# Performance work log

Hardware: AMD Instinct MI355X
Metric: run time of the kernel (lower is better)

Reference implementation:

```python
import jax, jax.numpy as jnp
import numpy as np

N, F, E, LIN, C, B = 16384, 500, 128, 128, 10, 4096
P_EDGE = 0.002  # ~32 avg degree


def _l2norm(x):
    # F.normalize(dim=1), eps=1e-12
    n = jnp.linalg.norm(x, axis=1, keepdims=True)
    return x / jnp.maximum(n, 1e-12)


def setup_inputs() -> dict:
    key = jax.random.key(0)
    ks = jax.random.split(key, 10)
    adj = (jax.random.uniform(ks[0], (N, N)) < P_EDGE).astype(jnp.float32)
    idx = jnp.arange(N)
    adj = adj.at[idx, idx].set(1.0)  # self-loops guarantee degree >= 1
    data = jax.random.normal(ks[1], (N, F), dtype=jnp.float32)
    nodes = jax.random.randint(ks[2], (B,), 0, N)
    # Encoder 1: Linear(2F -> E); Encoder 2: Linear(2E -> E); classifier heads
    W1 = jax.random.normal(ks[3], (E, 2 * F), dtype=jnp.float32) * 0.03
    b1 = jnp.zeros((E,), jnp.float32)
    W2 = jax.random.normal(ks[4], (E, 2 * E), dtype=jnp.float32) * 0.06
    b2 = jnp.zeros((E,), jnp.float32)
    Wl1 = jax.random.normal(ks[5], (LIN, E), dtype=jnp.float32) * 0.08
    bl1 = jnp.zeros((LIN,), jnp.float32)
    Wl2 = jax.random.normal(ks[6], (C, LIN), dtype=jnp.float32) * 0.12
    bl2 = jnp.zeros((C,), jnp.float32)
    return {"nodes": nodes, "adj": adj, "data": data,
            "W1": W1, "b1": b1, "W2": W2, "b2": b2,
            "Wl1": Wl1, "bl1": bl1, "Wl2": Wl2, "bl2": bl2}


def reference(nodes, adj, data, W1, b1, W2, b2, Wl1, bl1, Wl2, bl2):
    deg = jnp.sum(adj, axis=1, keepdims=True)  # [N,1]
    # Layer 1 (mean aggregator over full neighbor set): computed for all nodes
    neigh1 = (adj @ data) / deg                               # [N,F]
    h1 = jnp.concatenate([data, neigh1], axis=1)              # [N,2F] (self, neigh)
    H1 = _l2norm(jax.nn.relu(h1 @ W1.T + b1))                 # [N,E]
    # Layer 2: only for the queried node batch
    neigh2 = (adj[nodes] @ H1) / deg[nodes]                   # [B,E]
    h2 = jnp.concatenate([H1[nodes], neigh2], axis=1)         # [B,2E]
    H2 = _l2norm(jax.nn.relu(h2 @ W2.T + b2))                 # [B,E]
    x = H2 @ Wl1.T + bl1                                      # [B,LIN]
    x = x @ Wl2.T + bl2                                       # [B,C]
    return jax.nn.softmax(x, axis=1)
```

## Files before the change

### kernel.cpp

```cpp
#include <hip/hip_runtime.h>
#include <math.h>
#include <stddef.h>

#define N_NODES 16384
#define F_DIM   500
#define E_DIM   128
#define C_DIM   10
#define B_DIM   4096
#define MAXDEG  128

__global__ void k_prep_w1(const float* __restrict__ W1, float* __restrict__ W1s) {
    int idx = blockIdx.x * 256 + threadIdx.x;
    int e = idx & 255, k = idx >> 8;
    W1s[idx] = W1[(size_t)(e & 127) * 1000 + (e >> 7) * 500 + k];
}
__global__ void k_prep_w2(const float* __restrict__ W2, float* __restrict__ W2s) {
    int idx = blockIdx.x * 256 + threadIdx.x;
    int e = idx & 255, k = idx >> 8;
    W2s[idx] = W2[(size_t)(e & 127) * 256 + (e >> 7) * 128 + k];
}
__global__ void k_prep_wl1(const float* __restrict__ Wl1, float* __restrict__ Wl1t) {
    int idx = blockIdx.x * 256 + threadIdx.x;
    int e = idx & 127, k = idx >> 7;
    Wl1t[idx] = Wl1[(size_t)e * 128 + k];
}

__global__ __launch_bounds__(256) void k_gemm_s(const float* __restrict__ A, int K,
                                                const float* __restrict__ Bs,
                                                float* __restrict__ Cout) {
    __shared__ float sAT[32][36];
    __shared__ float sW[32][256];
    const int tid = threadIdx.x;
    const int c0 = (tid & 31) * 4;
    const int r0 = (tid >> 5) * 4;
    const int blockM = blockIdx.x * 32;
    const int kk_s = tid & 31;
    const int mm_s = tid >> 5;
    float acc[4][8] = {};

    for (int k0 = 0; k0 < K; k0 += 32) {
#pragma unroll
        for (int r = 0; r < 4; ++r) {
            int m = mm_s + r * 8;
            int k = k0 + kk_s;
            sAT[kk_s][m] = (k < K) ? A[(size_t)(blockM + m) * K + k] : 0.0f;
        }
#pragma unroll
        for (int q = 0; q < 8; ++q) {
            int idx4 = tid + 256 * q;
            int row = idx4 >> 6;
            int e4 = idx4 & 63;
            float4 w;
            if (k0 + row < K) w = ((const float4*)(Bs + (size_t)(k0 + row) * 256))[e4];
            else              w = make_float4(0.f, 0.f, 0.f, 0.f);
            *(float4*)&sW[row][e4 * 4] = w;
        }
        __syncthreads();
#pragma unroll 8
        for (int kk = 0; kk < 32; ++kk) {
            float4 a4 = *(const float4*)&sAT[kk][r0];
            float4 w0 = *(const float4*)&sW[kk][c0];
            float4 w1 = *(const float4*)&sW[kk][c0 + 128];
            float av[4] = {a4.x, a4.y, a4.z, a4.w};
            float wv[8] = {w0.x, w0.y, w0.z, w0.w, w1.x, w1.y, w1.z, w1.w};
#pragma unroll
            for (int i = 0; i < 4; ++i)
#pragma unroll
                for (int j = 0; j < 8; ++j)
                    acc[i][j] += av[i] * wv[j];
        }
        __syncthreads();
    }
#pragma unroll
    for (int i = 0; i < 4; ++i) {
        size_t base = (size_t)(blockM + r0 + i) * 256;
        *(float4*)&Cout[base + c0]       = make_float4(acc[i][0], acc[i][1], acc[i][2], acc[i][3]);
        *(float4*)&Cout[base + c0 + 128] = make_float4(acc[i][4], acc[i][5], acc[i][6], acc[i][7]);
    }
}

__global__ __launch_bounds__(256) void k_agg1(const float* __restrict__ adj,
                                              const float* __restrict__ X,
                                              const float* __restrict__ b1,
                                              float* __restrict__ H1,
                                              int* __restrict__ nbr,
                                              int* __restrict__ deg) {
    const int i = blockIdx.x;
    const int t = threadIdx.x;
    const float4* row4 = (const float4*)(adj + (size_t)i * N_NODES);
    __shared__ int s_cnt;
    __shared__ int s_idx[MAXDEG];
    __shared__ float s_part[2][128];
    __shared__ float s_w[2];
    if (t == 0) s_cnt = 0;
    __syncthreads();
    float4 v[16];
#pragma unroll
    for (int p = 0; p < 16; ++p) v[p] = row4[p * 256 + t];
#pragma unroll
    for (int p = 0; p < 16; ++p) {
        int col = p * 1024 + t * 4;
        if (v[p].x != 0.f) { int q = atomicAdd(&s_cnt, 1); if (q < MAXDEG) s_idx[q] = col;     }
        if (v[p].y != 0.f) { int q = atomicAdd(&s_cnt, 1); if (q < MAXDEG) s_idx[q] = col + 1; }
        if (v[p].z != 0.f) { int q = atomicAdd(&s_cnt, 1); if (q < MAXDEG) s_idx[q] = col + 2; }
        if (v[p].w != 0.f) { int q = atomicAdd(&s_cnt, 1); if (q < MAXDEG) s_idx[q] = col + 3; }
    }
    __syncthreads();
    int cnt = s_cnt; if (cnt > MAXDEG) cnt = MAXDEG;
    if (t < cnt) nbr[(size_t)i * MAXDEG + t] = s_idx[t];
    if (t == 0) deg[i] = cnt;
    const float inv = 1.0f / (float)cnt;
    const int col = t & 127;
    const int g = t >> 7;
    float acc = 0.f;
    for (int k = g; k < cnt; k += 2)
        acc += X[(size_t)s_idx[k] * 256 + 128 + col];
    s_part[g][col] = acc;
    __syncthreads();
    float vv = 0.f;
    if (t < 128) {
        float tot = s_part[0][t] + s_part[1][t];
        vv = X[(size_t)i * 256 + t] + tot * inv + b1[t];
        vv = fmaxf(vv, 0.f);
        float s = vv * vv;
#pragma unroll
        for (int off = 32; off > 0; off >>= 1) s += __shfl_down(s, off, 64);
        if ((t & 63) == 0) s_w[t >> 6] = s;
    }
    __syncthreads();
    if (t < 128) {
        float denom = fmaxf(sqrtf(s_w[0] + s_w[1]), 1e-12f);
        H1[(size_t)i * 128 + t] = vv / denom;
    }
}

__global__ __launch_bounds__(128) void k_l2head(const int* __restrict__ nodes,
                                                const int* __restrict__ nbr,
                                                const int* __restrict__ deg,
                                                const float* __restrict__ Y,
                                                const float* __restrict__ b2,
                                                const float* __restrict__ Wl1t,
                                                const float* __restrict__ bl1,
                                                const float* __restrict__ Wl2,
                                                const float* __restrict__ bl2,
                                                float* __restrict__ out) {
    const int b = blockIdx.x;
    const int t = threadIdx.x;
    const int n = nodes[b];
    const int cnt = deg[n];
    __shared__ int s_idx[MAXDEG];
    __shared__ float s_h[128];
    __shared__ float s_x[128];
    __shared__ float s_c[C_DIM];
    __shared__ float s_w[2];
    if (t < cnt) s_idx[t] = nbr[(size_t)n * MAXDEG + t];
    __syncthreads();
    float a0 = 0.f, a1 = 0.f;
    int k = 0;
    for (; k + 1 < cnt; k += 2) {
        a0 += Y[(size_t)s_idx[k]     * 256 + 128 + t];
        a1 += Y[(size_t)s_idx[k + 1] * 256 + 128 + t];
    }
    if (k < cnt) a0 += Y[(size_t)s_idx[k] * 256 + 128 + t];
    float vv = Y[(size_t)n * 256 + t] + (a0 + a1) / (float)cnt + b2[t];
    vv = fmaxf(vv, 0.f);
    float s = vv * vv;
#pragma unroll
    for (int off = 32; off > 0; off >>= 1) s += __shfl_down(s, off, 64);
    if ((t & 63) == 0) s_w[t >> 6] = s;
    __syncthreads();
    float denom = fmaxf(sqrtf(s_w[0] + s_w[1]), 1e-12f);
    s_h[t] = vv / denom;
    __syncthreads();
    float x1 = bl1[t];
#pragma unroll 8
    for (int kk = 0; kk < 128; ++kk)
        x1 += Wl1t[kk * 128 + t] * s_h[kk];
    s_x[t] = x1;
    __syncthreads();
    if (t < C_DIM) {
        float l = bl2[t];
        const float* wr = Wl2 + (size_t)t * 128;
        for (int kk = 0; kk < 128; ++kk) l += wr[kk] * s_x[kk];
        s_c[t] = l;
    }
    __syncthreads();
    if (t < C_DIM) {
        float mx = -1e30f;
        for (int c = 0; c < C_DIM; ++c) mx = fmaxf(mx, s_c[c]);
        float se = 0.f;
        for (int c = 0; c < C_DIM; ++c) se += expf(s_c[c] - mx);
        out[(size_t)b * C_DIM + t] = expf(s_c[t] - mx) / se;
    }
}

extern "C" void kernel_launch(void* const* d_in, const int* in_sizes, int n_in,
                              void* d_out, int out_size, void* d_ws, size_t ws_size,
                              hipStream_t stream) {
    const int*   nodes = (const int*)  d_in[0];
    const float* adj   = (const float*)d_in[1];
    const float* data  = (const float*)d_in[2];
    const float* W1    = (const float*)d_in[3];
    const float* b1    = (const float*)d_in[4];
    const float* W2    = (const float*)d_in[5];
    const float* b2    = (const float*)d_in[6];
    const float* Wl1   = (const float*)d_in[7];
    const float* bl1   = (const float*)d_in[8];
    const float* Wl2   = (const float*)d_in[9];
    const float* bl2   = (const float*)d_in[10];
    float* out = (float*)d_out;

    float* ws = (float*)d_ws;
    float* W1s  = ws;
    float* W2s  = W1s  + 128000;
    float* Wl1t = W2s  + 32768;
    float* X    = Wl1t + 16384;
    float* H1   = X    + 4194304;
    float* Y    = H1   + 2097152;
    int*   nbr  = (int*)(Y + 4194304);
    int*   deg  = nbr  + 16384 * MAXDEG;

    k_prep_w1 <<<500, 256, 0, stream>>>(W1, W1s);
    k_prep_w2 <<<128, 256, 0, stream>>>(W2, W2s);
    k_prep_wl1<<<64,  256, 0, stream>>>(Wl1, Wl1t);

    k_gemm_s<<<N_NODES / 32, 256, 0, stream>>>(data, F_DIM, W1s, X);
    k_agg1  <<<N_NODES, 256, 0, stream>>>(adj, X, b1, H1, nbr, deg);

    k_gemm_s<<<N_NODES / 32, 256, 0, stream>>>(H1, E_DIM, W2s, Y);
    k_l2head<<<B_DIM, 128, 0, stream>>>(nodes, nbr, deg, Y, b2, Wl1t, bl1, Wl2, bl2, out);
}
```

Measured before the change: 1.530 ms.

## Register-prefetch GEMM with larger 64-row tiles and tiled weight transposes

The weight-shuffle prep kernels are replaced by a shared-memory tiled transpose kernel launched per weight slice, so both reads and writes are coalesced. The shared GEMM now computes 64 rows per block with an 8x8 per-thread tile. It prefetches the next K chunk into registers while computing the current one, hiding global load latency behind FMAs. This raises register pressure and halves the block count.

```diff
diff --git a/kernel.cpp b/kernel.cpp
--- a/kernel.cpp
+++ b/kernel.cpp
@@ -9,70 +9,97 @@
 #define B_DIM   4096
 #define MAXDEG  128
 
-__global__ void k_prep_w1(const float* __restrict__ W1, float* __restrict__ W1s) {
-    int idx = blockIdx.x * 256 + threadIdx.x;
-    int e = idx & 255, k = idx >> 8;
-    W1s[idx] = W1[(size_t)(e & 127) * 1000 + (e >> 7) * 500 + k];
-}
-__global__ void k_prep_w2(const float* __restrict__ W2, float* __restrict__ W2s) {
-    int idx = blockIdx.x * 256 + threadIdx.x;
-    int e = idx & 255, k = idx >> 8;
-    W2s[idx] = W2[(size_t)(e & 127) * 256 + (e >> 7) * 128 + k];
-}
-__global__ void k_prep_wl1(const float* __restrict__ Wl1, float* __restrict__ Wl1t) {
-    int idx = blockIdx.x * 256 + threadIdx.x;
-    int e = idx & 127, k = idx >> 7;
-    Wl1t[idx] = Wl1[(size_t)e * 128 + k];
+__global__ void k_tp(const float* __restrict__ src, float* __restrict__ dst,
+                     int srcStride, int cOff, int Kc, int eOff, int dstStride) {
+    __shared__ float tile[32][33];
+    const int k0 = blockIdx.x * 32;
+    const int e0 = blockIdx.y * 32;
+    const int tx = threadIdx.x, ty0 = threadIdx.y;
+#pragma unroll
+    for (int q = 0; q < 4; ++q) {
+        int ty = ty0 + q * 8;
+        int k = k0 + tx;
+        tile[ty][tx] = (k < Kc) ? src[(size_t)(e0 + ty) * srcStride + cOff + k] : 0.0f;
+    }
+    __syncthreads();
+#pragma unroll
+    for (int q = 0; q < 4; ++q) {
+        int ty = ty0 + q * 8;
+        int k = k0 + ty;
+        if (k < Kc) dst[(size_t)k * dstStride + eOff + e0 + tx] = tile[tx][ty];
+    }
 }
 
 __global__ __launch_bounds__(256) void k_gemm_s(const float* __restrict__ A, int K,
                                                 const float* __restrict__ Bs,
                                                 float* __restrict__ Cout) {
-    __shared__ float sAT[32][36];
+    __shared__ float sAT[32][68];
     __shared__ float sW[32][256];
     const int tid = threadIdx.x;
     const int c0 = (tid & 31) * 4;
-    const int r0 = (tid >> 5) * 4;
-    const int blockM = blockIdx.x * 32;
+    const int r0 = (tid >> 5) * 8;
+    const int blockM = blockIdx.x * 64;
     const int kk_s = tid & 31;
-    const int mm_s = tid >> 5;
-    float acc[4][8] = {};
-
-    for (int k0 = 0; k0 < K; k0 += 32) {
-#pragma unroll
-        for (int r = 0; r < 4; ++r) {
-            int m = mm_s + r * 8;
-            int k = k0 + kk_s;
-            sAT[kk_s][m] = (k < K) ? A[(size_t)(blockM + m) * K + k] : 0.0f;
-        }
+    const int mg_s = (tid >> 5) * 8;
+    float acc[8][8] = {};
+    float  pa[8];
+    float4 pw[8];
+
+    const int nch = (K + 31) >> 5;
+
+    auto loadG = [&](int k0) {
+        int k = k0 + kk_s;
+#pragma unroll
+        for (int r = 0; r < 8; ++r)
+            pa[r] = (k < K) ? A[(size_t)(blockM + mg_s + r) * K + k] : 0.0f;
 #pragma unroll
         for (int q = 0; q < 8; ++q) {
             int idx4 = tid + 256 * q;
-            int row = idx4 >> 6;
-            int e4 = idx4 & 63;
-            float4 w;
-            if (k0 + row < K) w = ((const float4*)(Bs + (size_t)(k0 + row) * 256))[e4];
-            else              w = make_float4(0.f, 0.f, 0.f, 0.f);
-            *(float4*)&sW[row][e4 * 4] = w;
-        }
-        __syncthreads();
+            int row = idx4 >> 6, e4 = idx4 & 63;
+            pw[q] = (k0 + row < K) ? ((const float4*)(Bs + (size_t)(k0 + row) * 256))[e4]
+                                   : make_float4(0.f, 0.f, 0.f, 0.f);
+        }
+    };
+    auto storeL = [&]() {
+#pragma unroll
+        for (int r = 0; r < 8; ++r) sAT[kk_s][mg_s + r] = pa[r];
+#pragma unroll
+        for (int q = 0; q < 8; ++q) {
+            int idx4 = tid + 256 * q;
+            int row = idx4 >> 6, e4 = idx4 & 63;
+            *(float4*)&sW[row][e4 * 4] = pw[q];
+        }
+    };
+
+    loadG(0);
+    storeL();
+    __syncthreads();
+
+    for (int c = 1; c <= nch; ++c) {
+        const bool more = (c < nch);
+        if (more) loadG(c * 32);
 #pragma unroll 8
         for (int kk = 0; kk < 32; ++kk) {
-            float4 a4 = *(const float4*)&sAT[kk][r0];
+            float4 a0 = *(const float4*)&sAT[kk][r0];
+            float4 a1 = *(const float4*)&sAT[kk][r0 + 4];
             float4 w0 = *(const float4*)&sW[kk][c0];
             float4 w1 = *(const float4*)&sW[kk][c0 + 128];
-            float av[4] = {a4.x, a4.y, a4.z, a4.w};
+            float av[8] = {a0.x, a0.y, a0.z, a0.w, a1.x, a1.y, a1.z, a1.w};
             float wv[8] = {w0.x, w0.y, w0.z, w0.w, w1.x, w1.y, w1.z, w1.w};
 #pragma unroll
-            for (int i = 0; i < 4; ++i)
+            for (int i = 0; i < 8; ++i)
 #pragma unroll
                 for (int j = 0; j < 8; ++j)
                     acc[i][j] += av[i] * wv[j];
         }
-        __syncthreads();
-    }
-#pragma unroll
-    for (int i = 0; i < 4; ++i) {
+        if (more) {
+            __syncthreads();
+            storeL();
+            __syncthreads();
+        }
+    }
+#pragma unroll
+    for (int i = 0; i < 8; ++i) {
         size_t base = (size_t)(blockM + r0 + i) * 256;
         *(float4*)&Cout[base + c0]       = make_float4(acc[i][0], acc[i][1], acc[i][2], acc[i][3]);
         *(float4*)&Cout[base + c0 + 128] = make_float4(acc[i][4], acc[i][5], acc[i][6], acc[i][7]);
@@ -220,13 +247,16 @@
     int*   nbr  = (int*)(Y + 4194304);
     int*   deg  = nbr  + 16384 * MAXDEG;
 
-    k_prep_w1 <<<500, 256, 0, stream>>>(W1, W1s);
-    k_prep_w2 <<<128, 256, 0, stream>>>(W2, W2s);
-    k_prep_wl1<<<64,  256, 0, stream>>>(Wl1, Wl1t);
-
-    k_gemm_s<<<N_NODES / 32, 256, 0, stream>>>(data, F_DIM, W1s, X);
+    dim3 tpb(32, 8);
+    k_tp<<<dim3(16, 4), tpb, 0, stream>>>(W1, W1s, 1000, 0,   500, 0,   256);
+    k_tp<<<dim3(16, 4), tpb, 0, stream>>>(W1, W1s, 1000, 500, 500, 128, 256);
+    k_tp<<<dim3(4, 4),  tpb, 0, stream>>>(W2, W2s, 256,  0,   128, 0,   256);
+    k_tp<<<dim3(4, 4),  tpb, 0, stream>>>(W2, W2s, 256,  128, 128, 128, 256);
+    k_tp<<<dim3(4, 4),  tpb, 0, stream>>>(Wl1, Wl1t, 128, 0,  128, 0,   128);
+
+    k_gemm_s<<<N_NODES / 64, 256, 0, stream>>>(data, F_DIM, W1s, X);
     k_agg1  <<<N_NODES, 256, 0, stream>>>(adj, X, b1, H1, nbr, deg);
 
-    k_gemm_s<<<N_NODES / 32, 256, 0, stream>>>(H1, E_DIM, W2s, Y);
+    k_gemm_s<<<N_NODES / 64, 256, 0, stream>>>(H1, E_DIM, W2s, Y);
     k_l2head<<<B_DIM, 128, 0, stream>>>(nodes, nbr, deg, Y, b2, Wl1t, bl1, Wl2, bl2, out);
 }
```

Result: no change. 1.504 ms (-1.7%).

## Run layer GEMMs with bf16 MFMA and store H1 in bf16

Applied to the files above, without the earlier changes.

Replaces the fp32 scalar shared-memory GEMM with a bf16 MFMA 16x16x32 kernel. Input features are cast and padded to K=512, and weights are pre-transposed to bf16. H1 is written as bf16 to feed the second GEMM. This lowers GEMM compute and traffic but adds a cast pass and reduces precision of the intermediate activations.

```diff
diff --git a/kernel.cpp b/kernel.cpp
--- a/kernel.cpp
+++ b/kernel.cpp
@@ -4,85 +4,129 @@
 
 #define N_NODES 16384
 #define F_DIM   500
+#define KP1     512
 #define E_DIM   128
 #define C_DIM   10
 #define B_DIM   4096
 #define MAXDEG  128
 
-__global__ void k_prep_w1(const float* __restrict__ W1, float* __restrict__ W1s) {
+typedef __attribute__((ext_vector_type(8))) short short8;
+typedef __attribute__((ext_vector_type(4))) float f32x4;
+
+__device__ inline unsigned short f2bf(float f) {
+    union { float f; unsigned int u; } v; v.f = f;
+    unsigned int u = v.u;
+    u += 0x7FFFu + ((u >> 16) & 1u);
+    return (unsigned short)(u >> 16);
+}
+
+__global__ __launch_bounds__(256) void k_cast_data(const float* __restrict__ src,
+                                                   unsigned short* __restrict__ dst) {
     int idx = blockIdx.x * 256 + threadIdx.x;
-    int e = idx & 255, k = idx >> 8;
-    W1s[idx] = W1[(size_t)(e & 127) * 1000 + (e >> 7) * 500 + k];
-}
-__global__ void k_prep_w2(const float* __restrict__ W2, float* __restrict__ W2s) {
+    int i = idx >> 8, k2 = (idx & 255) * 2;
+    unsigned short a = 0, b = 0;
+    if (k2 < F_DIM) {
+        float2 d = *(const float2*)(src + (size_t)i * F_DIM + k2);
+        a = f2bf(d.x); b = f2bf(d.y);
+    }
+    ushort2 o; o.x = a; o.y = b;
+    *(ushort2*)(dst + (size_t)i * KP1 + k2) = o;
+}
+
+__global__ __launch_bounds__(256) void k_prep_w1b(const float* __restrict__ W1,
+                                                  unsigned short* __restrict__ Wt) {
     int idx = blockIdx.x * 256 + threadIdx.x;
-    int e = idx & 255, k = idx >> 8;
-    W2s[idx] = W2[(size_t)(e & 127) * 256 + (e >> 7) * 128 + k];
-}
-__global__ void k_prep_wl1(const float* __restrict__ Wl1, float* __restrict__ Wl1t) {
+    int n = idx >> 9, k = idx & 511;
+    float v = (k < F_DIM) ? W1[(size_t)(n & 127) * 1000 + (n >> 7) * F_DIM + k] : 0.0f;
+    Wt[idx] = f2bf(v);
+}
+
+__global__ __launch_bounds__(256) void k_prep_w2b(const float* __restrict__ W2,
+                                                  unsigned short* __restrict__ Wt) {
     int idx = blockIdx.x * 256 + threadIdx.x;
-    int e = idx & 127, k = idx >> 7;
-    Wl1t[idx] = Wl1[(size_t)e * 128 + k];
-}
-
-__global__ __launch_bounds__(256) void k_gemm_s(const float* __restrict__ A, int K,
-                                                const float* __restrict__ Bs,
-                                                float* __restrict__ Cout) {
-    __shared__ float sAT[32][36];
-    __shared__ float sW[32][256];
-    const int tid = threadIdx.x;
-    const int c0 = (tid & 31) * 4;
-    const int r0 = (tid >> 5) * 4;
+    int n = idx >> 7, k = idx & 127;
+    Wt[idx] = f2bf(W2[(size_t)(n & 127) * 256 + (n >> 7) * 128 + k]);
+}
+
+__global__ void k_tp(const float* __restrict__ src, float* __restrict__ dst) {
+    __shared__ float tile[32][33];
+    const int k0 = blockIdx.x * 32;
+    const int e0 = blockIdx.y * 32;
+    const int tx = threadIdx.x, ty0 = threadIdx.y;
+#pragma unroll
+    for (int q = 0; q < 4; ++q) {
+        int ty = ty0 + q * 8;
+        tile[ty][tx] = src[(size_t)(e0 + ty) * 128 + k0 + tx];
+    }
+    __syncthreads();
+#pragma unroll
+    for (int q = 0; q < 4; ++q) {
+        int ty = ty0 + q * 8;
+        dst[(size_t)(k0 + ty) * 128 + e0 + tx] = tile[tx][ty];
+    }
+}
+
+__global__ __launch_bounds__(256) void k_gemm_mfma(const unsigned short* __restrict__ A,
+                                                   const unsigned short* __restrict__ B,
+                                                   int K,
+                                                   float* __restrict__ Cout) {
+    __shared__ unsigned short sA[32 * 40];
+    __shared__ unsigned short sB[256 * 40];
+    const int tid  = threadIdx.x;
+    const int w    = tid >> 6;
+    const int lane = tid & 63;
+    const int l16  = lane & 15;
+    const int quad = lane >> 4;
     const int blockM = blockIdx.x * 32;
-    const int kk_s = tid & 31;
-    const int mm_s = tid >> 5;
-    float acc[4][8] = {};
-
-    for (int k0 = 0; k0 < K; k0 += 32) {
-#pragma unroll
-        for (int r = 0; r < 4; ++r) {
-            int m = mm_s + r * 8;
-            int k = k0 + kk_s;
-            sAT[kk_s][m] = (k < K) ? A[(size_t)(blockM + m) * K + k] : 0.0f;
+    f32x4 acc[2][4] = {};
+    const int nchunks = K >> 5;
+
+    for (int c = 0; c < nchunks; ++c) {
+        const int k0 = c << 5;
+        if (tid < 128) {
+            int row = tid >> 2, cc = tid & 3;
+            short8 v = *(const short8*)(A + (size_t)(blockM + row) * K + k0 + cc * 8);
+            *(short8*)(sA + row * 40 + cc * 8) = v;
         }
 #pragma unroll
-        for (int q = 0; q < 8; ++q) {
-            int idx4 = tid + 256 * q;
-            int row = idx4 >> 6;
-            int e4 = idx4 & 63;
-            float4 w;
-            if (k0 + row < K) w = ((const float4*)(Bs + (size_t)(k0 + row) * 256))[e4];
-            else              w = make_float4(0.f, 0.f, 0.f, 0.f);
-            *(float4*)&sW[row][e4 * 4] = w;
+        for (int q = 0; q < 4; ++q) {
+            int idx = tid + 256 * q;
+            int row = idx >> 2, cc = idx & 3;
+            short8 v = *(const short8*)(B + (size_t)row * K + k0 + cc * 8);
+            *(short8*)(sB + row * 40 + cc * 8) = v;
         }
         __syncthreads();
-#pragma unroll 8
-        for (int kk = 0; kk < 32; ++kk) {
-            float4 a4 = *(const float4*)&sAT[kk][r0];
-            float4 w0 = *(const float4*)&sW[kk][c0];
-            float4 w1 = *(const float4*)&sW[kk][c0 + 128];
-            float av[4] = {a4.x, a4.y, a4.z, a4.w};
-            float wv[8] = {w0.x, w0.y, w0.z, w0.w, w1.x, w1.y, w1.z, w1.w};
-#pragma unroll
-            for (int i = 0; i < 4; ++i)
-#pragma unroll
-                for (int j = 0; j < 8; ++j)
-                    acc[i][j] += av[i] * wv[j];
+        short8 af[2], bf[4];
+#pragma unroll
+        for (int mt = 0; mt < 2; ++mt)
+            af[mt] = *(const short8*)(sA + (mt * 16 + l16) * 40 + quad * 8);
+#pragma unroll
+        for (int nt = 0; nt < 4; ++nt)
+            bf[nt] = *(const short8*)(sB + (w * 64 + nt * 16 + l16) * 40 + quad * 8);
+#pragma unroll
+        for (int mt = 0; mt < 2; ++mt)
+#pragma unroll
+            for (int nt = 0; nt < 4; ++nt)
+                acc[mt][nt] = __builtin_amdgcn_mfma_f32_16x16x32_bf16(af[mt], bf[nt], acc[mt][nt], 0, 0, 0);
+        __syncthreads();
+    }
+#pragma unroll
+    for (int mt = 0; mt < 2; ++mt)
+#pragma unroll
+        for (int nt = 0; nt < 4; ++nt) {
+            int col = w * 64 + nt * 16 + l16;
+#pragma unroll
+            for (int r = 0; r < 4; ++r) {
+                int row = blockM + mt * 16 + quad * 4 + r;
+                Cout[(size_t)row * 256 + col] = acc[mt][nt][r];
+            }
         }
-        __syncthreads();
-    }
-#pragma unroll
-    for (int i = 0; i < 4; ++i) {
-        size_t base = (size_t)(blockM + r0 + i) * 256;
-        *(float4*)&Cout[base + c0]       = make_float4(acc[i][0], acc[i][1], acc[i][2], acc[i][3]);
-        *(float4*)&Cout[base + c0 + 128] = make_float4(acc[i][4], acc[i][5], acc[i][6], acc[i][7]);
-    }
 }
 
 __global__ __launch_bounds__(256) void k_agg1(const float* __restrict__ adj,
                                               const float* __restrict__ X,
                                               const float* __restrict__ b1,
-                                              float* __restrict__ H1,
+                                              unsigned short* __restrict__ H1b,
                                               int* __restrict__ nbr,
                                               int* __restrict__ deg) {
     const int i = blockIdx.x;
@@ -130,7 +174,7 @@
     __syncthreads();
     if (t < 128) {
         float denom = fmaxf(sqrtf(s_w[0] + s_w[1]), 1e-12f);
-        H1[(size_t)i * 128 + t] = vv / denom;
+        H1b[(size_t)i * 128 + t] = f2bf(vv / denom);
     }
 }
 
@@ -210,23 +254,24 @@
     const float* bl2   = (const float*)d_in[10];
     float* out = (float*)d_out;
 
-    float* ws = (float*)d_ws;
-    float* W1s  = ws;
-    float* W2s  = W1s  + 128000;
-    float* Wl1t = W2s  + 32768;
-    float* X    = Wl1t + 16384;
-    float* H1   = X    + 4194304;
-    float* Y    = H1   + 2097152;
-    int*   nbr  = (int*)(Y + 4194304);
-    int*   deg  = nbr  + 16384 * MAXDEG;
-
-    k_prep_w1 <<<500, 256, 0, stream>>>(W1, W1s);
-    k_prep_w2 <<<128, 256, 0, stream>>>(W2, W2s);
-    k_prep_wl1<<<64,  256, 0, stream>>>(Wl1, Wl1t);
-
-    k_gemm_s<<<N_NODES / 32, 256, 0, stream>>>(data, F_DIM, W1s, X);
-    k_agg1  <<<N_NODES, 256, 0, stream>>>(adj, X, b1, H1, nbr, deg);
-
-    k_gemm_s<<<N_NODES / 32, 256, 0, stream>>>(H1, E_DIM, W2s, Y);
-    k_l2head<<<B_DIM, 128, 0, stream>>>(nodes, nbr, deg, Y, b2, Wl1t, bl1, Wl2, bl2, out);
-}
+    unsigned short* Ab  = (unsigned short*)d_ws;
+    unsigned short* Wt1 = Ab  + (size_t)N_NODES * KP1;
+    unsigned short* Wt2 = Wt1 + 256 * KP1;
+    unsigned short* H1b = Wt2 + 256 * 128;
+    float* Wl1t = (float*)(H1b + (size_t)N_NODES * 128);
+    float* X    = Wl1t + 128 * 128;
+    float* Y    = X    + (size_t)N_NODES * 256;
+    int*   nbr  = (int*)(Y + (size_t)N_NODES * 256);
+    int*   deg  = nbr + (size_t)N_NODES * MAXDEG;
+
+    k_cast_data<<<N_NODES, 256, 0, stream>>>(data, Ab);
+    k_prep_w1b <<<512, 256, 0, stream>>>(W1, Wt1);
+    k_prep_w2b <<<128, 256, 0, stream>>>(W2, Wt2);
+    k_tp<<<dim3(4, 4), dim3(32, 8), 0, stream>>>(Wl1, Wl1t);
+
+    k_gemm_mfma<<<N_NODES / 32, 256, 0, stream>>>(Ab, Wt1, KP1, X);
+    k_agg1     <<<N_NODES, 256, 0, stream>>>(adj, X, b1, H1b, nbr, deg);
+
+    k_gemm_mfma<<<N_NODES / 32, 256, 0, stream>>>(H1b, Wt2, E_DIM, Y);
+    k_l2head   <<<B_DIM, 128, 0, stream>>>(nodes, nbr, deg, Y, b2, Wl1t, bl1, Wl2, bl2, out);
+}
```

After: 1.443 ms. -5.7%, faster.
